# Performance work log

Measured on AMD Instinct MI355X. Metric: run time of the kernel, lower is better.

Reference implementation:

```python
import jax, jax.numpy as jnp
import numpy as np

B, S, H, E = 4096, 200, 128, 64


def setup_inputs() -> dict:
    key = jax.random.key(0)
    ks = jax.random.split(key, 10)
    s = 0.05  # small init scale for weight matrices
    return {
        "interest_states": jax.random.normal(ks[0], (B, S, H), jnp.float32),
        "target_item": jax.random.normal(ks[1], (B, E), jnp.float32),
        "W_bil": jax.random.normal(ks[2], (H, E), jnp.float32) * s,
        "Wxu": jax.random.normal(ks[3], (H, H), jnp.float32) * s,
        "Whu": jax.random.normal(ks[4], (H, H), jnp.float32) * s,
        "bu": jnp.zeros((H,), jnp.float32),
        "Wxr": jax.random.normal(ks[5], (H, H), jnp.float32) * s,
        "Whr": jax.random.normal(ks[6], (H, H), jnp.float32) * s,
        "br": jnp.zeros((H,), jnp.float32),
        "Wxc": jax.random.normal(ks[7], (H, H), jnp.float32) * s,
        "Whc": jax.random.normal(ks[8], (H, H), jnp.float32) * s,
        "bc": jnp.zeros((H,), jnp.float32),
    }


def reference(interest_states, target_item, W_bil, Wxu, Whu, bu, Wxr, Whr, br, Wxc, Whc, bc):
    # Bilinear attention: a_t = softmax_t(h_t W e_a)  -> [B, S]
    logits = jnp.einsum('bsh,he,be->bs', interest_states, W_bil, target_item)
    att = jax.nn.softmax(logits, axis=1)

    def step(h, xs):
        x, a = xs  # x: [B, H], a: [B]
        u = jax.nn.sigmoid(x @ Wxu + h @ Whu + bu)          # update gate
        r = jax.nn.sigmoid(x @ Wxr + h @ Whr + br)          # reset gate
        c = jnp.tanh(x @ Wxc + (r * h) @ Whc + bc)          # candidate
        au = a[:, None] * u                                  # attention-scaled update gate
        h_new = (1.0 - au) * h + au * c
        return h_new, None

    h0 = jnp.zeros((interest_states.shape[0], Wxu.shape[1]), interest_states.dtype)
    xs = (jnp.swapaxes(interest_states, 0, 1), att.T)  # time-major: [S,B,H], [S,B]
    h_final, _ = jax.lax.scan(step, h0, xs)
    return h_final  # [B, H]
```

## Files before the change

### kernel.cpp

```cpp
#include <hip/hip_runtime.h>

typedef __attribute__((ext_vector_type(8))) short short8;
typedef __attribute__((ext_vector_type(4))) short short4v;
typedef __attribute__((ext_vector_type(4))) float float4v;

#define Hh 128
#define Ss 200
#define Ee 64
#define BR 16
#define TPB3 512

#if defined(__has_builtin) && __has_builtin(__builtin_amdgcn_exp2f)
#define EXP2F(x) __builtin_amdgcn_exp2f(x)
#else
#define EXP2F(x) exp2f(x)
#endif
#if defined(__has_builtin) && __has_builtin(__builtin_amdgcn_rcpf)
#define RCPF(x) __builtin_amdgcn_rcpf(x)
#else
#define RCPF(x) (1.0f / (x))
#endif

#define LOG2E 1.442695040888963f

__device__ __forceinline__ float fsig(float z) {
    return RCPF(1.0f + EXP2F(-LOG2E * z));
}
__device__ __forceinline__ float ftanh(float z) {
    return 1.0f - 2.0f * RCPF(1.0f + EXP2F(2.0f * LOG2E * z));
}

__device__ __forceinline__ short f2bf(float f) {
    unsigned u = __float_as_uint(f);
    u += 0x7FFFu + ((u >> 16) & 1u);
    return (short)(u >> 16);
}
__device__ __forceinline__ float bf2f(short s) {
    return __uint_as_float(((unsigned)(unsigned short)s) << 16);
}

__global__ __launch_bounds__(256) void v_kernel(
    const float* __restrict__ tgt, const float* __restrict__ Wb, float* __restrict__ v)
{
    __shared__ float tg[8][64];
    int tid = threadIdx.x;
    int b0 = blockIdx.x * 8;
    for (int i = tid; i < 8 * 64; i += 256) tg[i >> 6][i & 63] = tgt[(size_t)b0 * Ee + i];
    __syncthreads();

    int h = tid & 127, half = tid >> 7;
    float acc[4] = {0.f, 0.f, 0.f, 0.f};
    #pragma unroll
    for (int e4 = 0; e4 < 16; ++e4) {
        float4v wv = *(const float4v*)&Wb[h * Ee + e4 * 4];
        #pragma unroll
        for (int o = 0; o < 4; ++o) {
            float4v tv = *(const float4v*)&tg[half * 4 + o][e4 * 4];
            acc[o] += wv.x * tv.x + wv.y * tv.y + wv.z * tv.z + wv.w * tv.w;
        }
    }
    #pragma unroll
    for (int o = 0; o < 4; ++o)
        v[(size_t)(b0 + half * 4 + o) * Hh + h] = acc[o];
}

__global__ __launch_bounds__(256) void attn_kernel(
    const float* __restrict__ x, const float* __restrict__ v, float* __restrict__ att)
{
    __shared__ float vS[128];
    __shared__ float lg[256];
    __shared__ float redM, redZ;

    int tid = threadIdx.x;
    int b = blockIdx.x;

    if (tid < 128) vS[tid] = v[(size_t)b * Hh + tid];
    __syncthreads();

    float dot = 0.f;
    if (tid < Ss) {
        const float* xr = x + ((size_t)b * Ss + tid) * Hh;
        #pragma unroll 8
        for (int e4 = 0; e4 < 32; ++e4) {
            float4v xv = *(const float4v*)&xr[e4 * 4];
            dot += xv.x * vS[e4 * 4] + xv.y * vS[e4 * 4 + 1]
                 + xv.z * vS[e4 * 4 + 2] + xv.w * vS[e4 * 4 + 3];
        }
        lg[tid] = dot;
    }
    __syncthreads();

    if (tid < 64) {
        float m = -1e30f;
        for (int s = tid; s < Ss; s += 64) m = fmaxf(m, lg[s]);
        #pragma unroll
        for (int off = 32; off > 0; off >>= 1) m = fmaxf(m, __shfl_xor(m, off));
        float z = 0.f;
        for (int s = tid; s < Ss; s += 64) z += EXP2F((lg[s] - m) * LOG2E);
        #pragma unroll
        for (int off = 32; off > 0; off >>= 1) z += __shfl_xor(z, off);
        if (tid == 0) { redM = m; redZ = RCPF(z); }
    }
    __syncthreads();

    if (tid < Ss)
        att[(size_t)b * Ss + tid] = EXP2F((dot - redM) * LOG2E) * redZ;
}

__global__ __launch_bounds__(TPB3) void gru_kernel(
    const float* __restrict__ x, const float* __restrict__ att,
    const float* __restrict__ Wxu, const float* __restrict__ Whu, const float* __restrict__ bu,
    const float* __restrict__ Wxr, const float* __restrict__ Whr, const float* __restrict__ br,
    const float* __restrict__ Wxc, const float* __restrict__ Whc, const float* __restrict__ bc,
    float* __restrict__ out)
{
    __shared__ __align__(16) short xh[BR][264];
    __shared__ __align__(16) short rhs[BR][136];
    __shared__ __align__(16) float G1[BR][132];
    __shared__ __align__(16) float C2[BR][132];
    __shared__ float attS[BR][Ss];

    int tid = threadIdx.x;
    int wave = tid >> 6, lane = tid & 63;
    int quad = lane >> 4, l16 = lane & 15;
    int b0 = blockIdx.x * BR;

    short8 W1[2][8];
    short8 W2[8];
    #pragma unroll
    for (int t = 0; t < 2; ++t) {
        int fullcol = wave * 32 + t * 16 + l16;
        const float* Wx = (fullcol < 128) ? Wxu : Wxr;
        const float* Wh = (fullcol < 128) ? Whu : Whr;
        int n = fullcol & 127;
        #pragma unroll
        for (int q = 0; q < 8; ++q) {
            short8 f;
            #pragma unroll
            for (int j = 0; j < 8; ++j) {
                int k = q * 32 + quad * 8 + j;
                float wv = (k < 128) ? Wx[k * Hh + n] : Wh[(k - 128) * Hh + n];
                f[j] = f2bf(wv);
            }
            W1[t][q] = f;
        }
    }
    {
        int n2 = wave * 16 + l16;
        #pragma unroll
        for (int q = 0; q < 8; ++q) {
            short8 f;
            #pragma unroll
            for (int j = 0; j < 8; ++j) {
                int k = q * 32 + quad * 8 + j;
                float wv = (k < 128) ? Wxc[k * Hh + n2] : Whc[(k - 128) * Hh + n2];
                f[j] = f2bf(wv);
            }
            W2[q] = f;
        }
    }
    float b1[2];
    #pragma unroll
    for (int t = 0; t < 2; ++t) {
        int fullcol = wave * 32 + t * 16 + l16;
        b1[t] = (fullcol < 128) ? bu[fullcol] : br[fullcol - 128];
    }
    float b2 = bc[wave * 16 + l16];

    for (int i = tid; i < BR * Ss; i += TPB3) {
        int rr = i / Ss, sc = i % Ss;
        attS[rr][sc] = att[(size_t)(b0 + rr) * Ss + sc];
    }

    int urow = tid >> 5;
    int uc = (tid & 31) * 4;
    float hreg[4] = {0.f, 0.f, 0.f, 0.f};
    { short4v z = {0, 0, 0, 0}; *(short4v*)&xh[urow][128 + uc] = z; }

    const float* xrow = x + (size_t)(b0 + urow) * Ss * Hh + uc;
    float4v xv = *(const float4v*)&xrow[0];
    float4v xvn = xv;

    #pragma unroll 1
    for (int t = 0; t < Ss; ++t) {
        {
            short4v xs;
            #pragma unroll
            for (int i = 0; i < 4; ++i) xs[i] = f2bf(xv[i]);
            *(short4v*)&xh[urow][uc] = xs;
        }
        if (t + 1 < Ss) xvn = *(const float4v*)&xrow[(size_t)(t + 1) * Hh];
        __syncthreads();

        float4v a0 = {0.f, 0.f, 0.f, 0.f}, a1 = {0.f, 0.f, 0.f, 0.f};
        #pragma unroll
        for (int q = 0; q < 8; ++q) {
            short8 af = *(const short8*)&xh[l16][q * 32 + quad * 8];
            a0 = __builtin_amdgcn_mfma_f32_16x16x32_bf16(af, W1[0][q], a0, 0, 0, 0);
            a1 = __builtin_amdgcn_mfma_f32_16x16x32_bf16(af, W1[1][q], a1, 0, 0, 0);
        }
        if (wave < 4) {
            int c0 = wave * 32 + l16;
            #pragma unroll
            for (int r = 0; r < 4; ++r) {
                int rr = quad * 4 + r;
                G1[rr][c0]      = fsig(a0[r] + b1[0]);
                G1[rr][c0 + 16] = fsig(a1[r] + b1[1]);
            }
        } else {
            int c0 = (wave - 4) * 32 + l16;
            #pragma unroll
            for (int r = 0; r < 4; ++r) {
                int rr = quad * 4 + r;
                float r0 = fsig(a0[r] + b1[0]);
                float r1 = fsig(a1[r] + b1[1]);
                float h0 = bf2f(xh[rr][128 + c0]);
                float h1 = bf2f(xh[rr][128 + c0 + 16]);
                rhs[rr][c0]      = f2bf(r0 * h0);
                rhs[rr][c0 + 16] = f2bf(r1 * h1);
            }
        }
        __syncthreads();

        float4v a2 = {0.f, 0.f, 0.f, 0.f};
        #pragma unroll
        for (int q = 0; q < 4; ++q) {
            short8 af = *(const short8*)&xh[l16][q * 32 + quad * 8];
            a2 = __builtin_amdgcn_mfma_f32_16x16x32_bf16(af, W2[q], a2, 0, 0, 0);
        }
        #pragma unroll
        for (int q = 0; q < 4; ++q) {
            short8 af = *(const short8*)&rhs[l16][q * 32 + quad * 8];
            a2 = __builtin_amdgcn_mfma_f32_16x16x32_bf16(af, W2[q + 4], a2, 0, 0, 0);
        }
        {
            int c0 = wave * 16 + l16;
            #pragma unroll
            for (int r = 0; r < 4; ++r)
                C2[quad * 4 + r][c0] = ftanh(a2[r] + b2);
        }
        __syncthreads();

        {
            float a = attS[urow][t];
            short4v hv;
            #pragma unroll
            for (int i = 0; i < 4; ++i) {
                float u = G1[urow][uc + i];
                float c = C2[urow][uc + i];
                float au = a * u;
                hreg[i] = (1.f - au) * hreg[i] + au * c;
                hv[i] = f2bf(hreg[i]);
            }
            *(short4v*)&xh[urow][128 + uc] = hv;
        }
        xv = xvn;
    }

    float4v o;
    #pragma unroll
    for (int i = 0; i < 4; ++i) o[i] = hreg[i];
    *(float4v*)&out[(size_t)(b0 + urow) * Hh + uc] = o;
}

extern "C" void kernel_launch(void* const* d_in, const int* in_sizes, int n_in,
                              void* d_out, int out_size, void* d_ws, size_t ws_size,
                              hipStream_t stream) {
    const float* x   = (const float*)d_in[0];
    const float* tgt = (const float*)d_in[1];
    const float* Wb  = (const float*)d_in[2];
    const float* Wxu = (const float*)d_in[3];
    const float* Whu = (const float*)d_in[4];
    const float* bu  = (const float*)d_in[5];
    const float* Wxr = (const float*)d_in[6];
    const float* Whr = (const float*)d_in[7];
    const float* br  = (const float*)d_in[8];
    const float* Wxc = (const float*)d_in[9];
    const float* Whc = (const float*)d_in[10];
    const float* bc  = (const float*)d_in[11];
    float* out = (float*)d_out;

    const int B = in_sizes[1] / Ee;
    float* att = (float*)d_ws;
    float* v   = att + (size_t)B * Ss;

    v_kernel<<<B / 8, 256, 0, stream>>>(tgt, Wb, v);
    attn_kernel<<<B, 256, 0, stream>>>(x, v, att);
    gru_kernel<<<B / BR, TPB3, 0, stream>>>(x, att, Wxu, Whu, bu,
                                            Wxr, Whr, br, Wxc, Whc, bc, out);
}
```

Measured before the change: 845.4 us.

## Halve GRU batch tile to 8 rows, fuse v into attention, coalesce logits

The GRU kernel now handles 8 batch rows per block instead of 16, which doubles the grid to 512 blocks so more CUs stay busy during the long sequential recurrence. The MFMA tiles stay 16 rows wide with the upper half zero-padded, so half of the matrix work is wasted. The separate v_kernel is folded into the attention kernel, and the logit dot products now use 16-lane groups with shuffle reductions so x reads are coalesced. A launch-bounds occupancy hint is also added.

```diff
diff --git a/kernel.cpp b/kernel.cpp
--- a/kernel.cpp
+++ b/kernel.cpp
@@ -1,13 +1,14 @@
 #include <hip/hip_runtime.h>
 
 typedef __attribute__((ext_vector_type(8))) short short8;
-typedef __attribute__((ext_vector_type(4))) short short4v;
+typedef __attribute__((ext_vector_type(2))) short short2v;
 typedef __attribute__((ext_vector_type(4))) float float4v;
+typedef __attribute__((ext_vector_type(2))) float float2v;
 
 #define Hh 128
 #define Ss 200
 #define Ee 64
-#define BR 16
+#define BR 8
 #define TPB3 512
 
 #if defined(__has_builtin) && __has_builtin(__builtin_amdgcn_exp2f)
@@ -39,54 +40,50 @@
     return __uint_as_float(((unsigned)(unsigned short)s) << 16);
 }
 
-__global__ __launch_bounds__(256) void v_kernel(
-    const float* __restrict__ tgt, const float* __restrict__ Wb, float* __restrict__ v)
+__global__ __launch_bounds__(256) void attn_kernel(
+    const float* __restrict__ x, const float* __restrict__ tgt,
+    const float* __restrict__ Wb, float* __restrict__ att)
 {
-    __shared__ float tg[8][64];
-    int tid = threadIdx.x;
-    int b0 = blockIdx.x * 8;
-    for (int i = tid; i < 8 * 64; i += 256) tg[i >> 6][i & 63] = tgt[(size_t)b0 * Ee + i];
-    __syncthreads();
-
-    int h = tid & 127, half = tid >> 7;
-    float acc[4] = {0.f, 0.f, 0.f, 0.f};
-    #pragma unroll
-    for (int e4 = 0; e4 < 16; ++e4) {
-        float4v wv = *(const float4v*)&Wb[h * Ee + e4 * 4];
-        #pragma unroll
-        for (int o = 0; o < 4; ++o) {
-            float4v tv = *(const float4v*)&tg[half * 4 + o][e4 * 4];
-            acc[o] += wv.x * tv.x + wv.y * tv.y + wv.z * tv.z + wv.w * tv.w;
-        }
-    }
-    #pragma unroll
-    for (int o = 0; o < 4; ++o)
-        v[(size_t)(b0 + half * 4 + o) * Hh + h] = acc[o];
-}
-
-__global__ __launch_bounds__(256) void attn_kernel(
-    const float* __restrict__ x, const float* __restrict__ v, float* __restrict__ att)
-{
-    __shared__ float vS[128];
-    __shared__ float lg[256];
+    __shared__ float tgS[Ee];
+    __shared__ float vS[Hh];
+    __shared__ float lg[Ss];
     __shared__ float redM, redZ;
 
     int tid = threadIdx.x;
     int b = blockIdx.x;
 
-    if (tid < 128) vS[tid] = v[(size_t)b * Hh + tid];
-    __syncthreads();
-
-    float dot = 0.f;
-    if (tid < Ss) {
-        const float* xr = x + ((size_t)b * Ss + tid) * Hh;
-        #pragma unroll 8
-        for (int e4 = 0; e4 < 32; ++e4) {
-            float4v xv = *(const float4v*)&xr[e4 * 4];
-            dot += xv.x * vS[e4 * 4] + xv.y * vS[e4 * 4 + 1]
-                 + xv.z * vS[e4 * 4 + 2] + xv.w * vS[e4 * 4 + 3];
-        }
-        lg[tid] = dot;
+    if (tid < Ee) tgS[tid] = tgt[(size_t)b * Ee + tid];
+    __syncthreads();
+
+    if (tid < Hh) {
+        const float* wr = Wb + (size_t)tid * Ee;
+        float acc = 0.f;
+        #pragma unroll
+        for (int e4 = 0; e4 < Ee / 4; ++e4) {
+            float4v wv = *(const float4v*)&wr[e4 * 4];
+            float4v tv = *(const float4v*)&tgS[e4 * 4];
+            acc += wv.x * tv.x + wv.y * tv.y + wv.z * tv.z + wv.w * tv.w;
+        }
+        vS[tid] = acc;
+    }
+    __syncthreads();
+
+    int g = tid >> 4, l16 = tid & 15;
+    float v0[8];
+    #pragma unroll
+    for (int j = 0; j < 8; ++j) v0[j] = vS[l16 * 8 + j];
+
+    for (int s = g; s < Ss; s += 16) {
+        const float* xr = x + ((size_t)b * Ss + s) * Hh + l16 * 8;
+        float4v x0 = *(const float4v*)xr;
+        float4v x1 = *(const float4v*)(xr + 4);
+        float d = x0.x * v0[0] + x0.y * v0[1] + x0.z * v0[2] + x0.w * v0[3]
+                + x1.x * v0[4] + x1.y * v0[5] + x1.z * v0[6] + x1.w * v0[7];
+        d += __shfl_xor(d, 8);
+        d += __shfl_xor(d, 4);
+        d += __shfl_xor(d, 2);
+        d += __shfl_xor(d, 1);
+        if (l16 == 0) lg[s] = d;
     }
     __syncthreads();
 
@@ -104,18 +101,18 @@
     __syncthreads();
 
     if (tid < Ss)
-        att[(size_t)b * Ss + tid] = EXP2F((dot - redM) * LOG2E) * redZ;
-}
-
-__global__ __launch_bounds__(TPB3) void gru_kernel(
+        att[(size_t)b * Ss + tid] = EXP2F((lg[tid] - redM) * LOG2E) * redZ;
+}
+
+__global__ __launch_bounds__(TPB3, 4) void gru_kernel(
     const float* __restrict__ x, const float* __restrict__ att,
     const float* __restrict__ Wxu, const float* __restrict__ Whu, const float* __restrict__ bu,
     const float* __restrict__ Wxr, const float* __restrict__ Whr, const float* __restrict__ br,
     const float* __restrict__ Wxc, const float* __restrict__ Whc, const float* __restrict__ bc,
     float* __restrict__ out)
 {
-    __shared__ __align__(16) short xh[BR][264];
-    __shared__ __align__(16) short rhs[BR][136];
+    __shared__ __align__(16) short xh[16][264];
+    __shared__ __align__(16) short rhs[16][136];
     __shared__ __align__(16) float G1[BR][132];
     __shared__ __align__(16) float C2[BR][132];
     __shared__ float attS[BR][Ss];
@@ -167,29 +164,32 @@
     }
     float b2 = bc[wave * 16 + l16];
 
+    for (int i = tid; i < 8 * 264; i += TPB3) xh[8 + i / 264][i % 264] = 0;
+    for (int i = tid; i < 8 * 136; i += TPB3) rhs[8 + i / 136][i % 136] = 0;
+    for (int i = tid; i < 8 * 128; i += TPB3) xh[i >> 7][Hh + (i & 127)] = 0;
+
     for (int i = tid; i < BR * Ss; i += TPB3) {
         int rr = i / Ss, sc = i % Ss;
         attS[rr][sc] = att[(size_t)(b0 + rr) * Ss + sc];
     }
 
-    int urow = tid >> 5;
-    int uc = (tid & 31) * 4;
-    float hreg[4] = {0.f, 0.f, 0.f, 0.f};
-    { short4v z = {0, 0, 0, 0}; *(short4v*)&xh[urow][128 + uc] = z; }
+    int urow = tid >> 6;
+    int uc = (tid & 63) * 2;
+    float hreg[2] = {0.f, 0.f};
 
     const float* xrow = x + (size_t)(b0 + urow) * Ss * Hh + uc;
-    float4v xv = *(const float4v*)&xrow[0];
-    float4v xvn = xv;
+    float2v xv = *(const float2v*)xrow;
+    float2v xvn = xv;
 
     #pragma unroll 1
     for (int t = 0; t < Ss; ++t) {
         {
-            short4v xs;
-            #pragma unroll
-            for (int i = 0; i < 4; ++i) xs[i] = f2bf(xv[i]);
-            *(short4v*)&xh[urow][uc] = xs;
-        }
-        if (t + 1 < Ss) xvn = *(const float4v*)&xrow[(size_t)(t + 1) * Hh];
+            short2v xs;
+            xs[0] = f2bf(xv.x);
+            xs[1] = f2bf(xv.y);
+            *(short2v*)&xh[urow][uc] = xs;
+        }
+        if (t + 1 < Ss) xvn = *(const float2v*)&xrow[(size_t)(t + 1) * Hh];
         __syncthreads();
 
         float4v a0 = {0.f, 0.f, 0.f, 0.f}, a1 = {0.f, 0.f, 0.f, 0.f};
@@ -199,25 +199,27 @@
             a0 = __builtin_amdgcn_mfma_f32_16x16x32_bf16(af, W1[0][q], a0, 0, 0, 0);
             a1 = __builtin_amdgcn_mfma_f32_16x16x32_bf16(af, W1[1][q], a1, 0, 0, 0);
         }
-        if (wave < 4) {
-            int c0 = wave * 32 + l16;
-            #pragma unroll
-            for (int r = 0; r < 4; ++r) {
-                int rr = quad * 4 + r;
-                G1[rr][c0]      = fsig(a0[r] + b1[0]);
-                G1[rr][c0 + 16] = fsig(a1[r] + b1[1]);
-            }
-        } else {
-            int c0 = (wave - 4) * 32 + l16;
-            #pragma unroll
-            for (int r = 0; r < 4; ++r) {
-                int rr = quad * 4 + r;
-                float r0 = fsig(a0[r] + b1[0]);
-                float r1 = fsig(a1[r] + b1[1]);
-                float h0 = bf2f(xh[rr][128 + c0]);
-                float h1 = bf2f(xh[rr][128 + c0 + 16]);
-                rhs[rr][c0]      = f2bf(r0 * h0);
-                rhs[rr][c0 + 16] = f2bf(r1 * h1);
+        if (quad < 2) {
+            if (wave < 4) {
+                int c0 = wave * 32 + l16;
+                #pragma unroll
+                for (int r = 0; r < 4; ++r) {
+                    int rr = quad * 4 + r;
+                    G1[rr][c0]      = fsig(a0[r] + b1[0]);
+                    G1[rr][c0 + 16] = fsig(a1[r] + b1[1]);
+                }
+            } else {
+                int c0 = (wave - 4) * 32 + l16;
+                #pragma unroll
+                for (int r = 0; r < 4; ++r) {
+                    int rr = quad * 4 + r;
+                    float r0 = fsig(a0[r] + b1[0]);
+                    float r1 = fsig(a1[r] + b1[1]);
+                    float h0 = bf2f(xh[rr][Hh + c0]);
+                    float h1 = bf2f(xh[rr][Hh + c0 + 16]);
+                    rhs[rr][c0]      = f2bf(r0 * h0);
+                    rhs[rr][c0 + 16] = f2bf(r1 * h1);
+                }
             }
         }
         __syncthreads();
@@ -233,7 +235,7 @@
             short8 af = *(const short8*)&rhs[l16][q * 32 + quad * 8];
             a2 = __builtin_amdgcn_mfma_f32_16x16x32_bf16(af, W2[q + 4], a2, 0, 0, 0);
         }
-        {
+        if (quad < 2) {
             int c0 = wave * 16 + l16;
             #pragma unroll
             for (int r = 0; r < 4; ++r)
@@ -243,24 +245,24 @@
 
         {
             float a = attS[urow][t];
-            short4v hv;
-            #pragma unroll
-            for (int i = 0; i < 4; ++i) {
-                float u = G1[urow][uc + i];
-                float c = C2[urow][uc + i];
-                float au = a * u;
-                hreg[i] = (1.f - au) * hreg[i] + au * c;
-                hv[i] = f2bf(hreg[i]);
-            }
-            *(short4v*)&xh[urow][128 + uc] = hv;
+            float2v g = *(const float2v*)&G1[urow][uc];
+            float2v c = *(const float2v*)&C2[urow][uc];
+            short2v hv;
+            float au0 = a * g.x;
+            hreg[0] = (1.f - au0) * hreg[0] + au0 * c.x;
+            hv[0] = f2bf(hreg[0]);
+            float au1 = a * g.y;
+            hreg[1] = (1.f - au1) * hreg[1] + au1 * c.y;
+            hv[1] = f2bf(hreg[1]);
+            *(short2v*)&xh[urow][Hh + uc] = hv;
         }
         xv = xvn;
     }
 
-    float4v o;
-    #pragma unroll
-    for (int i = 0; i < 4; ++i) o[i] = hreg[i];
-    *(float4v*)&out[(size_t)(b0 + urow) * Hh + uc] = o;
+    float2v o;
+    o.x = hreg[0];
+    o.y = hreg[1];
+    *(float2v*)&out[(size_t)(b0 + urow) * Hh + uc] = o;
 }
 
 extern "C" void kernel_launch(void* const* d_in, const int* in_sizes, int n_in,
@@ -282,10 +284,8 @@
 
     const int B = in_sizes[1] / Ee;
     float* att = (float*)d_ws;
-    float* v   = att + (size_t)B * Ss;
-
-    v_kernel<<<B / 8, 256, 0, stream>>>(tgt, Wb, v);
-    attn_kernel<<<B, 256, 0, stream>>>(x, v, att);
+
+    attn_kernel<<<B, 256, 0, stream>>>(x, tgt, Wb, att);
     gru_kernel<<<B / BR, TPB3, 0, stream>>>(x, att, Wxu, Whu, bu,
                                             Wxr, Whr, br, Wxc, Whc, bc, out);
 }
```

Result: slower. 1.201 ms (+42.0%).

## Fuse bilinear projection and attention softmax into the GRU kernel

Applied to the files above, without the earlier changes.

Removes the separate v and attention kernels and computes the bilinear vector, the logits and the softmax for the block's 16 rows inside the GRU kernel, with shared memory reused as scratch. This cuts two launches and the global round trip of att and v, though x is still read twice (once for the logits, once in the recurrence). The trade-off is a serial prologue per block of 256 blocks, which may pull more x from the L2 cache and hold back the start of the recurrence.

```diff
diff --git a/kernel.cpp b/kernel.cpp
--- a/kernel.cpp
+++ b/kernel.cpp
@@ -39,76 +39,9 @@
     return __uint_as_float(((unsigned)(unsigned short)s) << 16);
 }
 
-__global__ __launch_bounds__(256) void v_kernel(
-    const float* __restrict__ tgt, const float* __restrict__ Wb, float* __restrict__ v)
-{
-    __shared__ float tg[8][64];
-    int tid = threadIdx.x;
-    int b0 = blockIdx.x * 8;
-    for (int i = tid; i < 8 * 64; i += 256) tg[i >> 6][i & 63] = tgt[(size_t)b0 * Ee + i];
-    __syncthreads();
-
-    int h = tid & 127, half = tid >> 7;
-    float acc[4] = {0.f, 0.f, 0.f, 0.f};
-    #pragma unroll
-    for (int e4 = 0; e4 < 16; ++e4) {
-        float4v wv = *(const float4v*)&Wb[h * Ee + e4 * 4];
-        #pragma unroll
-        for (int o = 0; o < 4; ++o) {
-            float4v tv = *(const float4v*)&tg[half * 4 + o][e4 * 4];
-            acc[o] += wv.x * tv.x + wv.y * tv.y + wv.z * tv.z + wv.w * tv.w;
-        }
-    }
-    #pragma unroll
-    for (int o = 0; o < 4; ++o)
-        v[(size_t)(b0 + half * 4 + o) * Hh + h] = acc[o];
-}
-
-__global__ __launch_bounds__(256) void attn_kernel(
-    const float* __restrict__ x, const float* __restrict__ v, float* __restrict__ att)
-{
-    __shared__ float vS[128];
-    __shared__ float lg[256];
-    __shared__ float redM, redZ;
-
-    int tid = threadIdx.x;
-    int b = blockIdx.x;
-
-    if (tid < 128) vS[tid] = v[(size_t)b * Hh + tid];
-    __syncthreads();
-
-    float dot = 0.f;
-    if (tid < Ss) {
-        const float* xr = x + ((size_t)b * Ss + tid) * Hh;
-        #pragma unroll 8
-        for (int e4 = 0; e4 < 32; ++e4) {
-            float4v xv = *(const float4v*)&xr[e4 * 4];
-            dot += xv.x * vS[e4 * 4] + xv.y * vS[e4 * 4 + 1]
-                 + xv.z * vS[e4 * 4 + 2] + xv.w * vS[e4 * 4 + 3];
-        }
-        lg[tid] = dot;
-    }
-    __syncthreads();
-
-    if (tid < 64) {
-        float m = -1e30f;
-        for (int s = tid; s < Ss; s += 64) m = fmaxf(m, lg[s]);
-        #pragma unroll
-        for (int off = 32; off > 0; off >>= 1) m = fmaxf(m, __shfl_xor(m, off));
-        float z = 0.f;
-        for (int s = tid; s < Ss; s += 64) z += EXP2F((lg[s] - m) * LOG2E);
-        #pragma unroll
-        for (int off = 32; off > 0; off >>= 1) z += __shfl_xor(z, off);
-        if (tid == 0) { redM = m; redZ = RCPF(z); }
-    }
-    __syncthreads();
-
-    if (tid < Ss)
-        att[(size_t)b * Ss + tid] = EXP2F((dot - redM) * LOG2E) * redZ;
-}
-
-__global__ __launch_bounds__(TPB3) void gru_kernel(
-    const float* __restrict__ x, const float* __restrict__ att,
+__global__ __launch_bounds__(TPB3) void fused_kernel(
+    const float* __restrict__ x, const float* __restrict__ tgt,
+    const float* __restrict__ Wb,
     const float* __restrict__ Wxu, const float* __restrict__ Whu, const float* __restrict__ bu,
     const float* __restrict__ Wxr, const float* __restrict__ Whr, const float* __restrict__ br,
     const float* __restrict__ Wxc, const float* __restrict__ Whc, const float* __restrict__ bc,
@@ -125,6 +58,89 @@
     int quad = lane >> 4, l16 = lane & 15;
     int b0 = blockIdx.x * BR;
 
+    float* tg = &C2[0][0];
+    float* vv = &G1[0][0];
+
+    for (int i = tid; i < BR * Ee; i += TPB3) tg[i] = tgt[(size_t)b0 * Ee + i];
+    __syncthreads();
+
+    {
+        int h = tid & 127, rq = tid >> 7;
+        float acc[4] = {0.f, 0.f, 0.f, 0.f};
+        const float* wr = Wb + (size_t)h * Ee;
+        #pragma unroll
+        for (int e4 = 0; e4 < Ee / 4; ++e4) {
+            float4v wv = *(const float4v*)&wr[e4 * 4];
+            #pragma unroll
+            for (int ro = 0; ro < 4; ++ro) {
+                float4v tv = *(const float4v*)&tg[(rq * 4 + ro) * Ee + e4 * 4];
+                acc[ro] += wv.x * tv.x + wv.y * tv.y + wv.z * tv.z + wv.w * tv.w;
+            }
+        }
+        #pragma unroll
+        for (int ro = 0; ro < 4; ++ro) vv[(rq * 4 + ro) * Hh + h] = acc[ro];
+    }
+    __syncthreads();
+
+    #pragma unroll 1
+    for (int rr = 0; rr < 2; ++rr) {
+        int r = wave * 2 + rr;
+        float vr[8];
+        *(float4v*)&vr[0] = *(const float4v*)&vv[r * Hh + l16 * 8];
+        *(float4v*)&vr[4] = *(const float4v*)&vv[r * Hh + l16 * 8 + 4];
+        const float* xb = x + ((size_t)(b0 + r) * Ss) * Hh + l16 * 8;
+        for (int s0 = quad * 4; s0 < Ss; s0 += 16) {
+            float4v xa[4][2];
+            #pragma unroll
+            for (int j = 0; j < 4; ++j) {
+                const float* xr = xb + (size_t)(s0 + j) * Hh;
+                xa[j][0] = *(const float4v*)xr;
+                xa[j][1] = *(const float4v*)(xr + 4);
+            }
+            #pragma unroll
+            for (int j = 0; j < 4; ++j) {
+                float d = xa[j][0].x * vr[0] + xa[j][0].y * vr[1]
+                        + xa[j][0].z * vr[2] + xa[j][0].w * vr[3]
+                        + xa[j][1].x * vr[4] + xa[j][1].y * vr[5]
+                        + xa[j][1].z * vr[6] + xa[j][1].w * vr[7];
+                d += __shfl_xor(d, 8);
+                d += __shfl_xor(d, 4);
+                d += __shfl_xor(d, 2);
+                d += __shfl_xor(d, 1);
+                if (l16 == 0) attS[r][s0 + j] = d;
+            }
+        }
+    }
+    #pragma unroll 1
+    for (int rr = 0; rr < 2; ++rr) {
+        int r = wave * 2 + rr;
+        float vals[4], m = -1e30f;
+        #pragma unroll
+        for (int i = 0; i < 4; ++i) {
+            int s = lane + i * 64;
+            vals[i] = (s < Ss) ? attS[r][s] : -1e30f;
+            m = fmaxf(m, vals[i]);
+        }
+        #pragma unroll
+        for (int off = 32; off > 0; off >>= 1) m = fmaxf(m, __shfl_xor(m, off));
+        float z = 0.f;
+        #pragma unroll
+        for (int i = 0; i < 4; ++i) {
+            int s = lane + i * 64;
+            vals[i] = (s < Ss) ? EXP2F((vals[i] - m) * LOG2E) : 0.f;
+            z += vals[i];
+        }
+        #pragma unroll
+        for (int off = 32; off > 0; off >>= 1) z += __shfl_xor(z, off);
+        float zi = RCPF(z);
+        #pragma unroll
+        for (int i = 0; i < 4; ++i) {
+            int s = lane + i * 64;
+            if (s < Ss) attS[r][s] = vals[i] * zi;
+        }
+    }
+    __syncthreads();
+
     short8 W1[2][8];
     short8 W2[8];
     #pragma unroll
@@ -166,11 +182,6 @@
         b1[t] = (fullcol < 128) ? bu[fullcol] : br[fullcol - 128];
     }
     float b2 = bc[wave * 16 + l16];
-
-    for (int i = tid; i < BR * Ss; i += TPB3) {
-        int rr = i / Ss, sc = i % Ss;
-        attS[rr][sc] = att[(size_t)(b0 + rr) * Ss + sc];
-    }
 
     int urow = tid >> 5;
     int uc = (tid & 31) * 4;
@@ -281,11 +292,7 @@
     float* out = (float*)d_out;
 
     const int B = in_sizes[1] / Ee;
-    float* att = (float*)d_ws;
-    float* v   = att + (size_t)B * Ss;
-
-    v_kernel<<<B / 8, 256, 0, stream>>>(tgt, Wb, v);
-    attn_kernel<<<B, 256, 0, stream>>>(x, v, att);
-    gru_kernel<<<B / BR, TPB3, 0, stream>>>(x, att, Wxu, Whu, bu,
-                                            Wxr, Whr, br, Wxc, Whc, bc, out);
-}
+
+    fused_kernel<<<B / BR, TPB3, 0, stream>>>(x, tgt, Wb, Wxu, Whu, bu,
+                                              Wxr, Whr, br, Wxc, Whc, bc, out);
+}
```

New measurement: 833.6 us. No clear change (-1.4%).
